# Kernel tuning notes

Hardware: AMD Instinct MI355X
Metric: run time of the kernel (lower is better)

## Reference

```python
import jax, jax.numpy as jnp
import numpy as np

EPS = 1e-5
NUM_HEADS = 32

def layer_norm(x, g, b):
    m = jnp.mean(x, axis=-1, keepdims=True)
    v = jnp.mean((x - m) ** 2, axis=-1, keepdims=True)
    return (x - m) * jax.lax.rsqrt(v + EPS) * g + b

def positional_encoding(S, E):
    pos = jnp.arange(S, dtype=jnp.float32)[:, None]
    div = jnp.exp(jnp.arange(0, E, 2, dtype=jnp.float32) * (-jnp.log(10000.0) / E))
    ang = pos * div  # [S, E/2]
    pe = jnp.zeros((S, E), jnp.float32)
    pe = pe.at[:, 0::2].set(jnp.sin(ang)).at[:, 1::2].set(jnp.cos(ang))
    return pe

def quantum_attention(x, phi_l):
    # QLayer circuit: RX(x_j + phi_j) per wire, CNOT ring, measure Z.
    # Heisenberg picture: <Z_i> = prod_{j<=i} cos(a_j) for i>=1,
    #                     <Z_0> = prod_{j>=1} cos(a_j), a_j = x_j + phi_j.
    B, S, E = x.shape
    dk = E // NUM_HEADS  # = 8 wires
    c = jnp.cos(x.reshape(B, S, NUM_HEADS, dk) + phi_l)  # per-wire <Z> factor
    pref = jnp.cumprod(c, axis=-1)                       # prod_{j<=i}
    out0 = jnp.prod(c[..., 1:], axis=-1)                 # wire 0
    q = jnp.concatenate([out0[..., None], pref[..., 1:]], axis=-1)
    q = q.reshape(B, S, E)
    scores = jax.nn.softmax(
        jnp.einsum('bse,bte->bst', q, q) / jnp.sqrt(jnp.float32(dk)), axis=-1)
    return jnp.einsum('bst,bte->bse', scores, q)

def quantum_ffn(x, theta_l, W1_l, b1_l, W2_l, b2_l):
    # QLayer: RX(x_i) then RY(theta_i) on |0>, product state => <Z_i>=cos(x_i)cos(theta_i)
    nq = theta_l.shape[0]  # 8; encoder only reads first nq features
    qm = jnp.cos(x[..., :nq]) * jnp.cos(theta_l)
    h = jax.nn.relu(qm @ W1_l + b1_l)
    return h @ W2_l + b2_l

def setup_inputs() -> dict:
    key = jax.random.key(0)
    ks = jax.random.split(key, 10)
    V, E, L, FF, NQ, NC = 32000, 256, 4, 1024, 8, 10
    B, S = 8, 2048
    return {
        'tokens': jax.random.randint(ks[0], (B, S), 0, V, dtype=jnp.int64)
            if jax.config.jax_enable_x64 else jax.random.randint(ks[0], (B, S), 0, V, dtype=jnp.int32),
        'emb': jax.random.normal(ks[1], (V, E), jnp.float32),
        'phi': jax.random.normal(ks[2], (L, NQ), jnp.float32),
        'theta': jax.random.normal(ks[3], (L, NQ), jnp.float32),
        'W1': jax.random.normal(ks[4], (L, NQ, FF), jnp.float32) * 0.1,
        'b1': jax.random.normal(ks[5], (L, FF), jnp.float32) * 0.1,
        'W2': jax.random.normal(ks[6], (L, FF, E), jnp.float32) * 0.05,
        'b2': jax.random.normal(ks[7], (L, E), jnp.float32) * 0.05,
        'g1': jnp.ones((L, E), jnp.float32),
        'beta1': jnp.zeros((L, E), jnp.float32),
        'g2': jnp.ones((L, E), jnp.float32),
        'beta2': jnp.zeros((L, E), jnp.float32),
        'Wc': jax.random.normal(ks[8], (E, NC), jnp.float32) * 0.05,
        'bc': jax.random.normal(ks[9], (NC,), jnp.float32) * 0.05,
    }

def reference(tokens, emb, phi, theta, W1, b1, W2, b2, g1, beta1, g2, beta2, Wc, bc):
    B, S = tokens.shape
    E = emb.shape[1]
    x = emb[tokens] + positional_encoding(S, E)
    for l in range(phi.shape[0]):  # fixed num_blocks loop
        a = quantum_attention(x, phi[l])
        x = layer_norm(x + a, g1[l], beta1[l])
        f = quantum_ffn(x, theta[l], W1[l], b1[l], W2[l], b2[l])
        x = layer_norm(x + f, g2[l], beta2[l])
    return jnp.mean(x, axis=1) @ Wc + bc
```

## Files before the change

### kernel.cpp

```cpp
#include <hip/hip_runtime.h>
#include <hip/hip_bf16.h>

#define B_ 8
#define S_ 2048
#define E_ 256
#define FF_ 1024
#define NQ_ 8
#define NC_ 10
#define BS_ (B_*S_)
#define NSPLIT 2
#define KVBLK 32

typedef __bf16 bf16x8 __attribute__((ext_vector_type(8)));
typedef float f32x4 __attribute__((ext_vector_type(4)));

#define MFMA16(a,b,c) __builtin_amdgcn_mfma_f32_16x16x32_bf16(a,b,c,0,0,0)

__global__ __launch_bounds__(256) void k_embed(const int* __restrict__ tokens,
                                               const float* __restrict__ emb,
                                               float* __restrict__ x) {
    int row = blockIdx.x;
    int e = threadIdx.x;
    int s = row & (S_ - 1);
    int tok = tokens[row];
    int i2 = e & ~1;
    float d = __expf((float)i2 * (-9.210340371976184f / 256.0f));
    float ang = (float)s * d;
    float pe = (e & 1) ? __cosf(ang) : __sinf(ang);
    x[(size_t)row * E_ + e] = emb[(size_t)tok * E_ + e] + pe;
}

__global__ __launch_bounds__(256) void k_qt(const float* __restrict__ x,
                                            const float* __restrict__ phi_l,
                                            __hip_bfloat16* __restrict__ qbf,
                                            __hip_bfloat16* __restrict__ qT) {
    __shared__ __align__(16) __bf16 tile[64][76];
    int t0 = blockIdx.x * 64, e0 = blockIdx.y * 64, b = blockIdx.z;
    int tid = threadIdx.x;
    float ph[8];
#pragma unroll
    for (int j = 0; j < 8; j++) ph[j] = phi_l[j];
#pragma unroll
    for (int k = 0; k < 2; k++) {
        int idx = k * 256 + tid;
        int r = idx >> 3, hh = idx & 7;
        const float* xp = x + ((size_t)b * S_ + t0 + r) * E_ + e0 + hh * 8;
        f32x4 x0 = *(const f32x4*)xp;
        f32x4 x1 = *(const f32x4*)(xp + 4);
        float c[8];
#pragma unroll
        for (int j = 0; j < 4; j++) {
            c[j]     = __cosf(x0[j] + ph[j]);
            c[4 + j] = __cosf(x1[j] + ph[4 + j]);
        }
        float q[8];
        float run = c[0];
#pragma unroll
        for (int i = 1; i < 8; i++) { run *= c[i]; q[i] = run; }
        float o0 = c[1];
#pragma unroll
        for (int i = 2; i < 8; i++) o0 *= c[i];
        q[0] = o0;
        bf16x8 v;
#pragma unroll
        for (int j = 0; j < 8; j++) v[j] = (__bf16)q[j];
        *(bf16x8*)(qbf + ((size_t)b * S_ + t0 + r) * E_ + e0 + hh * 8) = v;
        *(bf16x8*)&tile[r][hh * 8] = v;
    }
    __syncthreads();
#pragma unroll
    for (int k = 0; k < 2; k++) {
        int idx = k * 256 + tid;
        int el = idx >> 3, tc = idx & 7;
        bf16x8 v;
#pragma unroll
        for (int j = 0; j < 8; j++) v[j] = tile[tc * 8 + j][el];
        *(bf16x8*)(qT + ((size_t)b * E_ + e0 + el) * S_ + t0 + tc * 8) = v;
    }
}

__global__ __launch_bounds__(256, 2) void k_attn(const __hip_bfloat16* __restrict__ qbf,
                                                 const __hip_bfloat16* __restrict__ qT,
                                                 float* __restrict__ pacc,
                                                 float* __restrict__ pl) {
    __shared__ __align__(16) __bf16 ktile[KVBLK * 256];
    __shared__ __align__(16) __bf16 vtile[256 * 36];
    __shared__ __align__(16) __bf16 plds[2][32][36];
    __shared__ float redl[2][32][2];
    const float SCALE = 0.3535533905932738f;
    int bid  = blockIdx.x;
    int b    = bid & 7;
    int qt   = (bid >> 3) & 31;
    int z    = bid >> 8;
    int tid  = threadIdx.x;
    int wv   = tid >> 6;
    int lane = tid & 63;
    int r16  = lane & 15;
    int kg   = lane >> 4;
    int rg   = wv >> 1, eh = wv & 1;
    int qrow0 = qt * 64 + rg * 32;
    int ebase = eh * 128;

    bf16x8 aq[2][8];
#pragma unroll
    for (int qs = 0; qs < 2; qs++)
#pragma unroll
        for (int kk = 0; kk < 8; kk++)
            aq[qs][kk] = *(const bf16x8*)(qbf + ((size_t)b * S_ + qrow0 + qs * 16 + r16) * E_ + kk * 32 + kg * 8);

    f32x4 acc0[8], acc1[8];
#pragma unroll
    for (int cf = 0; cf < 8; cf++) { acc0[cf] = (f32x4){0.f,0.f,0.f,0.f}; acc1[cf] = (f32x4){0.f,0.f,0.f,0.f}; }
    float lrow0[4] = {0.f,0.f,0.f,0.f}, lrow1[4] = {0.f,0.f,0.f,0.f};

    int k0 = z * (S_ / NSPLIT);
    const int NT = (S_ / NSPLIT) / KVBLK;
    bf16x8 vst[4];

    auto issue_k = [&](int kb) {
#pragma unroll
        for (int c = 0; c < 4; c++) {
            int seg = wv * 4 + c;
            int r = seg * 2 + (lane >> 5);
            int ch = lane & 31;
            const __hip_bfloat16* src = qbf + ((size_t)b * S_ + kb + r) * E_ + ((ch ^ (r & 7)) * 8);
            __builtin_amdgcn_global_load_lds((const __attribute__((address_space(1))) void*)src,
                                             (__attribute__((address_space(3))) void*)(ktile + seg * 512),
                                             16, 0, 0);
        }
    };
    auto issue_v = [&](int kb) {
#pragma unroll
        for (int p = 0; p < 4; p++) {
            int slot = p * 256 + tid;
            vst[p] = *(const bf16x8*)(qT + ((size_t)b * E_ + (slot >> 2)) * S_ + kb + (slot & 3) * 8);
        }
    };
    auto write_v = [&]() {
#pragma unroll
        for (int p = 0; p < 4; p++) {
            int slot = p * 256 + tid;
            *(bf16x8*)&vtile[(slot >> 2) * 36 + (slot & 3) * 8] = vst[p];
        }
    };

    issue_k(k0);
    issue_v(k0);
    asm volatile("s_waitcnt vmcnt(0)" ::: "memory");
    write_v();
    __syncthreads();

    for (int kt = 0; kt < NT; kt++) {
        f32x4 s0 = (f32x4){0.f,0.f,0.f,0.f}, s1 = (f32x4){0.f,0.f,0.f,0.f};
#pragma unroll
        for (int kk = 0; kk < 8; kk++) {
            bf16x8 bk = *(const bf16x8*)&ktile[(eh * 16 + r16) * 256 + (((kk * 4 + kg) ^ (r16 & 7)) * 8)];
            s0 = MFMA16(aq[0][kk], bk, s0);
            s1 = MFMA16(aq[1][kk], bk, s1);
        }
#pragma unroll
        for (int i = 0; i < 4; i++) {
            float p0 = __expf(fmaf(s0[i], SCALE, -44.0f));
            float p1 = __expf(fmaf(s1[i], SCALE, -44.0f));
            plds[rg][kg * 4 + i][eh * 16 + r16]      = (__bf16)p0;
            plds[rg][16 + kg * 4 + i][eh * 16 + r16] = (__bf16)p1;
            lrow0[i] += p0;
            lrow1[i] += p1;
        }
        __syncthreads();
        bool more = (kt + 1 < NT);
        if (more) {
            int kn = k0 + (kt + 1) * KVBLK;
            issue_k(kn);
            issue_v(kn);
        }
        bf16x8 pa0 = *(const bf16x8*)&plds[rg][r16][kg * 8];
        bf16x8 pa1 = *(const bf16x8*)&plds[rg][16 + r16][kg * 8];
#pragma unroll
        for (int cf = 0; cf < 8; cf++) {
            bf16x8 bv = *(const bf16x8*)&vtile[(ebase + cf * 16 + r16) * 36 + kg * 8];
            acc0[cf] = MFMA16(pa0, bv, acc0[cf]);
            acc1[cf] = MFMA16(pa1, bv, acc1[cf]);
        }
        if (more) {
            asm volatile("s_waitcnt vmcnt(0)" ::: "memory");
            __syncthreads();
            write_v();
        }
    }

#pragma unroll
    for (int i = 0; i < 4; i++) {
#pragma unroll
        for (int m = 1; m <= 8; m <<= 1) {
            lrow0[i] += __shfl_xor(lrow0[i], m);
            lrow1[i] += __shfl_xor(lrow1[i], m);
        }
    }
    if (r16 == 0) {
#pragma unroll
        for (int i = 0; i < 4; i++) {
            redl[rg][kg * 4 + i][eh]      = lrow0[i];
            redl[rg][16 + kg * 4 + i][eh] = lrow1[i];
        }
    }
    __syncthreads();
    size_t prow0 = (size_t)z * BS_ + (size_t)b * S_ + qrow0;
    if (eh == 0 && r16 == 0) {
#pragma unroll
        for (int i = 0; i < 4; i++) {
            int q = kg * 4 + i;
            pl[prow0 + q]      = redl[rg][q][0] + redl[rg][q][1];
            pl[prow0 + 16 + q] = redl[rg][16 + q][0] + redl[rg][16 + q][1];
        }
    }
#pragma unroll
    for (int i = 0; i < 4; i++) {
#pragma unroll
        for (int cf = 0; cf < 8; cf++) {
            pacc[(prow0 + kg * 4 + i) * E_ + ebase + cf * 16 + r16]      = acc0[cf][i];
            pacc[(prow0 + 16 + kg * 4 + i) * E_ + ebase + cf * 16 + r16] = acc1[cf][i];
        }
    }
}

__global__ __launch_bounds__(256) void k_aln(const float* __restrict__ pacc,
                                             const float* __restrict__ pl,
                                             float* __restrict__ x,
                                             const float* __restrict__ g,
                                             const float* __restrict__ bb) {
    int wv = threadIdx.x >> 6, lane = threadIdx.x & 63;
    size_t row = (size_t)blockIdx.x * 4 + wv;
    float inv = 1.0f / (pl[row] + pl[BS_ + row]);
    f32x4 a0 = ((const f32x4*)(pacc + row * E_))[lane];
    f32x4 a1 = ((const f32x4*)(pacc + (size_t)BS_ * E_ + row * E_))[lane];
    f32x4 xv = ((const f32x4*)(x + row * E_))[lane];
    f32x4 v;
    float s = 0.f, sq = 0.f;
#pragma unroll
    for (int j = 0; j < 4; j++) {
        v[j] = xv[j] + (a0[j] + a1[j]) * inv;
        s += v[j]; sq += v[j] * v[j];
    }
#pragma unroll
    for (int m = 1; m <= 32; m <<= 1) { s += __shfl_xor(s, m); sq += __shfl_xor(sq, m); }
    float mean = s * (1.f / E_);
    float var = sq * (1.f / E_) - mean * mean;
    float rstd = rsqrtf(var + 1e-5f);
    f32x4 gv = ((const f32x4*)g)[lane];
    f32x4 bv = ((const f32x4*)bb)[lane];
    f32x4 o;
#pragma unroll
    for (int j = 0; j < 4; j++) o[j] = (v[j] - mean) * rstd * gv[j] + bv[j];
    ((f32x4*)(x + row * E_))[lane] = o;
}

__global__ __launch_bounds__(256) void k_w2t(const float* __restrict__ W2l,
                                             __hip_bfloat16* __restrict__ w2t) {
    __shared__ __align__(16) __bf16 tile[64][72];
    int k0 = blockIdx.x * 64, e0 = blockIdx.y * 64;
    int tid = threadIdx.x;
#pragma unroll
    for (int half = 0; half < 2; half++) {
        int r  = half * 32 + (tid >> 3);
        int c8 = (tid & 7) * 8;
        f32x4 v0 = *(const f32x4*)(W2l + (size_t)(k0 + r) * E_ + e0 + c8);
        f32x4 v1 = *(const f32x4*)(W2l + (size_t)(k0 + r) * E_ + e0 + c8 + 4);
#pragma unroll
        for (int j = 0; j < 4; j++) { tile[r][c8 + j] = (__bf16)v0[j]; tile[r][c8 + 4 + j] = (__bf16)v1[j]; }
    }
    __syncthreads();
#pragma unroll
    for (int half = 0; half < 2; half++) {
        int e  = half * 32 + (tid >> 3);
        int k8 = (tid & 7) * 8;
        bf16x8 v;
#pragma unroll
        for (int j = 0; j < 8; j++) v[j] = tile[k8 + j][e];
        *(bf16x8*)(w2t + (size_t)(e0 + e) * FF_ + k0 + k8) = v;
    }
}

__global__ __launch_bounds__(256) void k_ffn(const float* __restrict__ x,
                                             const float* __restrict__ theta_l,
                                             const float* __restrict__ W1l,
                                             const float* __restrict__ b1l,
                                             const __hip_bfloat16* __restrict__ w2t,
                                             const float* __restrict__ b2l,
                                             const float* __restrict__ g,
                                             const float* __restrict__ bb) {
    __shared__ __align__(16) __bf16 Bld[2][256 * 64];
    __shared__ __align__(16) __bf16 Ald[2][32 * 64];
    __shared__ float qmld[32][9];
    __shared__ float reds[32][4][2];
    int tid = threadIdx.x;
    int wv = tid >> 6, lane = tid & 63;
    int r16 = lane & 15, kg = lane >> 4;
    int rbase = blockIdx.x * 32;
    int ebQ = wv * 64;
    const int NT = FF_ / 64;

    {
        int r = tid >> 3, i = tid & 7;
        qmld[r][i] = __cosf(x[(size_t)(rbase + r) * E_ + i]) * __cosf(theta_l[i]);
    }

    f32x4 w[18];

    auto issue_B = [&](int kt, int buf) {
#pragma unroll
        for (int s = 0; s < 8; s++) {
            int seg = wv * 8 + s;
            int e = seg * 8 + (lane >> 3);
            int c = lane & 7;
            const __hip_bfloat16* src = w2t + (size_t)e * FF_ + kt * 64 + ((c ^ (e & 7)) * 8);
            __builtin_amdgcn_global_load_lds((const __attribute__((address_space(1))) void*)src,
                                             (__attribute__((address_space(3))) void*)(&Bld[buf][seg * 512]),
                                             16, 0, 0);
        }
    };
    auto load_W1 = [&](int kt) {
        int c = tid & 7;
        int k = kt * 64 + c * 8;
#pragma unroll
        for (int i = 0; i < 8; i++) {
            w[2 * i]     = *(const f32x4*)(W1l + (size_t)i * FF_ + k);
            w[2 * i + 1] = *(const f32x4*)(W1l + (size_t)i * FF_ + k + 4);
        }
        w[16] = *(const f32x4*)(b1l + k);
        w[17] = *(const f32x4*)(b1l + k + 4);
    };
    auto math_h = [&](int buf) {
        int r = tid >> 3, c = tid & 7;
        f32x4 h0 = w[16], h1 = w[17];
#pragma unroll
        for (int i = 0; i < 8; i++) {
            float qv = qmld[r][i];
#pragma unroll
            for (int j = 0; j < 4; j++) {
                h0[j] = fmaf(qv, w[2 * i][j], h0[j]);
                h1[j] = fmaf(qv, w[2 * i + 1][j], h1[j]);
            }
        }
        bf16x8 hv;
#pragma unroll
        for (int j = 0; j < 4; j++) {
            hv[j]     = (__bf16)fmaxf(h0[j], 0.f);
            hv[4 + j] = (__bf16)fmaxf(h1[j], 0.f);
        }
        *(bf16x8*)&Ald[buf][r * 64 + ((c ^ (r & 7)) * 8)] = hv;
    };

    issue_B(0, 0);
    load_W1(0);
    __syncthreads();
    math_h(0);
    __syncthreads();

    f32x4 acc[2][4];
#pragma unroll
    for (int qs = 0; qs < 2; qs++)
#pragma unroll
        for (int cf = 0; cf < 4; cf++) acc[qs][cf] = (f32x4){0.f, 0.f, 0.f, 0.f};

    for (int kt = 0; kt < NT; kt++) {
        int cur = kt & 1;
        bool more = (kt + 1 < NT);
        if (more) {
            issue_B(kt + 1, cur ^ 1);
            load_W1(kt + 1);
        }
        bf16x8 aq[2][2];
#pragma unroll
        for (int qs = 0; qs < 2; qs++)
#pragma unroll
            for (int kk = 0; kk < 2; kk++)
                aq[qs][kk] = *(const bf16x8*)&Ald[cur][(qs * 16 + r16) * 64 + (((kk * 4 + kg) ^ (r16 & 7)) * 8)];
#pragma unroll
        for (int cf = 0; cf < 4; cf++) {
            int e = ebQ + cf * 16 + r16;
#pragma unroll
            for (int kk = 0; kk < 2; kk++) {
                bf16x8 bv = *(const bf16x8*)&Bld[cur][e * 64 + (((kk * 4 + kg) ^ (e & 7)) * 8)];
                acc[0][cf] = MFMA16(aq[0][kk], bv, acc[0][cf]);
                acc[1][cf] = MFMA16(aq[1][kk], bv, acc[1][cf]);
            }
        }
        if (more) {
            math_h(cur ^ 1);
            __syncthreads();
        }
    }

    float sA[2][4] = {{0.f,0.f,0.f,0.f},{0.f,0.f,0.f,0.f}};
    float sQ[2][4] = {{0.f,0.f,0.f,0.f},{0.f,0.f,0.f,0.f}};
#pragma unroll
    for (int qs = 0; qs < 2; qs++)
#pragma unroll
        for (int cf = 0; cf < 4; cf++) {
            int e = ebQ + cf * 16 + r16;
            float b2v = b2l[e];
#pragma unroll
            for (int i = 0; i < 4; i++) {
                size_t orow = (size_t)rbase + qs * 16 + kg * 4 + i;
                float t = acc[qs][cf][i] + b2v + x[orow * E_ + e];
                acc[qs][cf][i] = t;
                sA[qs][i] += t; sQ[qs][i] += t * t;
            }
        }
#pragma unroll
    for (int qs = 0; qs < 2; qs++)
#pragma unroll
        for (int i = 0; i < 4; i++) {
#pragma unroll
            for (int m = 1; m <= 8; m <<= 1) {
                sA[qs][i] += __shfl_xor(sA[qs][i], m);
                sQ[qs][i] += __shfl_xor(sQ[qs][i], m);
            }
        }
    if (r16 == 0) {
#pragma unroll
        for (int qs = 0; qs < 2; qs++)
#pragma unroll
            for (int i = 0; i < 4; i++) {
                int row = qs * 16 + kg * 4 + i;
                reds[row][wv][0] = sA[qs][i];
                reds[row][wv][1] = sQ[qs][i];
            }
    }
    __syncthreads();
    float mean[2][4], rstd[2][4];
#pragma unroll
    for (int qs = 0; qs < 2; qs++)
#pragma unroll
        for (int i = 0; i < 4; i++) {
            int row = qs * 16 + kg * 4 + i;
            float S = reds[row][0][0] + reds[row][1][0] + reds[row][2][0] + reds[row][3][0];
            float Q = reds[row][0][1] + reds[row][1][1] + reds[row][2][1] + reds[row][3][1];
            mean[qs][i] = S * (1.f / E_);
            float var = Q * (1.f / E_) - mean[qs][i] * mean[qs][i];
            rstd[qs][i] = rsqrtf(var + 1e-5f);
        }
    float* xo = (float*)x;
#pragma unroll
    for (int qs = 0; qs < 2; qs++)
#pragma unroll
        for (int cf = 0; cf < 4; cf++) {
            int e = ebQ + cf * 16 + r16;
            float gv = g[e], bv = bb[e];
#pragma unroll
            for (int i = 0; i < 4; i++) {
                size_t orow = (size_t)rbase + qs * 16 + kg * 4 + i;
                xo[orow * E_ + e] = (acc[qs][cf][i] - mean[qs][i]) * rstd[qs][i] * gv + bv;
            }
        }
}

__global__ __launch_bounds__(256) void k_mean(const float* __restrict__ x, float* __restrict__ psum) {
    int c = blockIdx.x, b = blockIdx.y, e = threadIdx.x;
    float s = 0.f;
    size_t base = ((size_t)b * S_ + c * 128) * E_ + e;
    for (int r = 0; r < 128; r++) s += x[base + (size_t)r * E_];
    psum[(c * 8 + b) * E_ + e] = s;
}

__global__ __launch_bounds__(256) void k_mean2(const float* __restrict__ psum, float* __restrict__ xmean) {
    int idx = blockIdx.x * 256 + threadIdx.x;
    int b = idx >> 8, e = idx & 255;
    float s = 0.f;
    for (int c = 0; c < 16; c++) s += psum[(c * 8 + b) * E_ + e];
    xmean[idx] = s * (1.f / S_);
}

__global__ __launch_bounds__(128) void k_cls(const float* __restrict__ xmean,
                                             const float* __restrict__ Wc,
                                             const float* __restrict__ bc,
                                             float* __restrict__ outp) {
    int t = threadIdx.x;
    if (t >= B_ * NC_) return;
    int b = t / NC_, c = t % NC_;
    float s = bc[c];
    for (int e = 0; e < E_; e++) s += xmean[b * E_ + e] * Wc[e * NC_ + c];
    outp[t] = s;
}

extern "C" void kernel_launch(void* const* d_in, const int* in_sizes, int n_in,
                              void* d_out, int out_size, void* d_ws, size_t ws_size,
                              hipStream_t stream) {
    (void)in_sizes; (void)n_in; (void)out_size; (void)ws_size;
    const int*   tokens = (const int*)d_in[0];
    const float* emb    = (const float*)d_in[1];
    const float* phi    = (const float*)d_in[2];
    const float* theta  = (const float*)d_in[3];
    const float* W1     = (const float*)d_in[4];
    const float* b1     = (const float*)d_in[5];
    const float* W2     = (const float*)d_in[6];
    const float* b2     = (const float*)d_in[7];
    const float* g1     = (const float*)d_in[8];
    const float* beta1  = (const float*)d_in[9];
    const float* g2     = (const float*)d_in[10];
    const float* beta2  = (const float*)d_in[11];
    const float* Wc     = (const float*)d_in[12];
    const float* bc     = (const float*)d_in[13];
    float* outp = (float*)d_out;

    float* xbuf = (float*)d_ws;
    __hip_bfloat16* qbf = (__hip_bfloat16*)(xbuf + (size_t)BS_ * E_);
    __hip_bfloat16* qT  = qbf + (size_t)BS_ * E_;
    __hip_bfloat16* w2t = qT + (size_t)BS_ * E_;
    float* psum  = (float*)(w2t + (size_t)E_ * FF_);
    float* xmean = psum + 16 * 8 * E_;
    float* pl    = xmean + B_ * E_;
    float* pacc  = pl + NSPLIT * BS_;

    k_embed<<<BS_, 256, 0, stream>>>(tokens, emb, xbuf);

    for (int l = 0; l < 4; l++) {
        k_qt<<<dim3(S_ / 64, E_ / 64, B_), 256, 0, stream>>>(xbuf, phi + l * NQ_, qbf, qT);
        k_attn<<<(S_ / 64) * B_ * NSPLIT, 256, 0, stream>>>(qbf, qT, pacc, pl);
        k_aln<<<BS_ / 4, 256, 0, stream>>>(pacc, pl, xbuf, g1 + l * E_, beta1 + l * E_);
        k_w2t<<<dim3(FF_ / 64, E_ / 64), 256, 0, stream>>>(W2 + (size_t)l * FF_ * E_, w2t);
        k_ffn<<<BS_ / 32, 256, 0, stream>>>(xbuf, theta + l * NQ_,
                                            W1 + (size_t)l * NQ_ * FF_, b1 + (size_t)l * FF_,
                                            w2t, b2 + (size_t)l * E_,
                                            g2 + l * E_, beta2 + l * E_);
    }

    k_mean<<<dim3(16, B_), 256, 0, stream>>>(xbuf, psum);
    k_mean2<<<8, 256, 0, stream>>>(psum, xmean);
    k_cls<<<1, 128, 0, stream>>>(xmean, Wc, bc, outp);
}
```

Baseline: 464.5 us.

## Make attention KV split count runtime-selectable and raise attention occupancy hint

The attention kernel now splits the key range into nz chunks chosen at runtime (4 when the workspace can hold the larger partial buffers, else 2), doubling the grid so more blocks are in flight. The add-layernorm kernel sums a variable number of partial accumulators and row sums. Launch bounds for attention go from 2 to 4 waves per SIMD, which caps registers per thread and may cause spills given the large accumulator arrays. More splits also mean more partial-result memory traffic in the combine step.

```diff
diff --git a/kernel.cpp b/kernel.cpp
--- a/kernel.cpp
+++ b/kernel.cpp
@@ -8,7 +8,6 @@
 #define NQ_ 8
 #define NC_ 10
 #define BS_ (B_*S_)
-#define NSPLIT 2
 #define KVBLK 32
 
 typedef __bf16 bf16x8 __attribute__((ext_vector_type(8)));
@@ -79,10 +78,11 @@
     }
 }
 
-__global__ __launch_bounds__(256, 2) void k_attn(const __hip_bfloat16* __restrict__ qbf,
+__global__ __launch_bounds__(256, 4) void k_attn(const __hip_bfloat16* __restrict__ qbf,
                                                  const __hip_bfloat16* __restrict__ qT,
                                                  float* __restrict__ pacc,
-                                                 float* __restrict__ pl) {
+                                                 float* __restrict__ pl,
+                                                 int nz) {
     __shared__ __align__(16) __bf16 ktile[KVBLK * 256];
     __shared__ __align__(16) __bf16 vtile[256 * 36];
     __shared__ __align__(16) __bf16 plds[2][32][36];
@@ -113,8 +113,9 @@
     for (int cf = 0; cf < 8; cf++) { acc0[cf] = (f32x4){0.f,0.f,0.f,0.f}; acc1[cf] = (f32x4){0.f,0.f,0.f,0.f}; }
     float lrow0[4] = {0.f,0.f,0.f,0.f}, lrow1[4] = {0.f,0.f,0.f,0.f};
 
-    int k0 = z * (S_ / NSPLIT);
-    const int NT = (S_ / NSPLIT) / KVBLK;
+    int span = S_ / nz;
+    int k0 = z * span;
+    int NT = span / KVBLK;
     bf16x8 vst[4];
 
     auto issue_k = [&](int kb) {
@@ -228,18 +229,25 @@
                                              const float* __restrict__ pl,
                                              float* __restrict__ x,
                                              const float* __restrict__ g,
-                                             const float* __restrict__ bb) {
+                                             const float* __restrict__ bb,
+                                             int nz) {
     int wv = threadIdx.x >> 6, lane = threadIdx.x & 63;
     size_t row = (size_t)blockIdx.x * 4 + wv;
-    float inv = 1.0f / (pl[row] + pl[BS_ + row]);
-    f32x4 a0 = ((const f32x4*)(pacc + row * E_))[lane];
-    f32x4 a1 = ((const f32x4*)(pacc + (size_t)BS_ * E_ + row * E_))[lane];
+    float lsum = 0.f;
+    for (int zi = 0; zi < nz; zi++) lsum += pl[(size_t)zi * BS_ + row];
+    float inv = 1.0f / lsum;
+    f32x4 a = (f32x4){0.f, 0.f, 0.f, 0.f};
+    for (int zi = 0; zi < nz; zi++) {
+        f32x4 av = ((const f32x4*)(pacc + (size_t)zi * BS_ * E_ + row * E_))[lane];
+#pragma unroll
+        for (int j = 0; j < 4; j++) a[j] += av[j];
+    }
     f32x4 xv = ((const f32x4*)(x + row * E_))[lane];
     f32x4 v;
     float s = 0.f, sq = 0.f;
 #pragma unroll
     for (int j = 0; j < 4; j++) {
-        v[j] = xv[j] + (a0[j] + a1[j]) * inv;
+        v[j] = xv[j] + a[j] * inv;
         s += v[j]; sq += v[j] * v[j];
     }
 #pragma unroll
@@ -487,7 +495,7 @@
 extern "C" void kernel_launch(void* const* d_in, const int* in_sizes, int n_in,
                               void* d_out, int out_size, void* d_ws, size_t ws_size,
                               hipStream_t stream) {
-    (void)in_sizes; (void)n_in; (void)out_size; (void)ws_size;
+    (void)in_sizes; (void)n_in; (void)out_size;
     const int*   tokens = (const int*)d_in[0];
     const float* emb    = (const float*)d_in[1];
     const float* phi    = (const float*)d_in[2];
@@ -504,6 +512,11 @@
     const float* bc     = (const float*)d_in[13];
     float* outp = (float*)d_out;
 
+    size_t fixed = (size_t)BS_ * E_ * 4 + (size_t)BS_ * E_ * 2 * 2 + (size_t)E_ * FF_ * 2
+                 + (size_t)16 * 8 * E_ * 4 + (size_t)B_ * E_ * 4;
+    size_t per_z = (size_t)BS_ * 4 + (size_t)BS_ * E_ * 4;
+    int nz = (ws_size >= fixed + 4 * per_z + 4096) ? 4 : 2;
+
     float* xbuf = (float*)d_ws;
     __hip_bfloat16* qbf = (__hip_bfloat16*)(xbuf + (size_t)BS_ * E_);
     __hip_bfloat16* qT  = qbf + (size_t)BS_ * E_;
@@ -511,14 +524,14 @@
     float* psum  = (float*)(w2t + (size_t)E_ * FF_);
     float* xmean = psum + 16 * 8 * E_;
     float* pl    = xmean + B_ * E_;
-    float* pacc  = pl + NSPLIT * BS_;
+    float* pacc  = pl + (size_t)nz * BS_;
 
     k_embed<<<BS_, 256, 0, stream>>>(tokens, emb, xbuf);
 
     for (int l = 0; l < 4; l++) {
         k_qt<<<dim3(S_ / 64, E_ / 64, B_), 256, 0, stream>>>(xbuf, phi + l * NQ_, qbf, qT);
-        k_attn<<<(S_ / 64) * B_ * NSPLIT, 256, 0, stream>>>(qbf, qT, pacc, pl);
-        k_aln<<<BS_ / 4, 256, 0, stream>>>(pacc, pl, xbuf, g1 + l * E_, beta1 + l * E_);
+        k_attn<<<(S_ / 64) * B_ * nz, 256, 0, stream>>>(qbf, qT, pacc, pl, nz);
+        k_aln<<<BS_ / 4, 256, 0, stream>>>(pacc, pl, xbuf, g1 + l * E_, beta1 + l * E_, nz);
         k_w2t<<<dim3(FF_ / 64, E_ / 64), 256, 0, stream>>>(W2 + (size_t)l * FF_ * E_, w2t);
         k_ffn<<<BS_ / 32, 256, 0, stream>>>(xbuf, theta + l * NQ_,
                                             W1 + (size_t)l * NQ_ * FF_, b1 + (size_t)l * FF_,
```

Result: slower. 1.256 ms (+170.3%).

## Fuse attention-combine layernorm into FFN kernel and async-load V tiles into LDS

Applied to the files above, without the earlier changes.

Removes the separate k_aln kernel. The FFN kernel now reads the two split-K attention partials and the row sums, adds the residual, applies the first layernorm in registers, and derives the quantum FFN input from the normalized values. This saves a full read/write pass over the activations and one launch per layer. Separately, k_attn loads V tiles through global_load_lds into double-buffered, XOR-swizzled LDS instead of staging them in registers. That frees VGPRs and removes the LDS write step, at the cost of more shared memory per block, which may reduce occupancy.

```diff
diff --git a/kernel.cpp b/kernel.cpp
--- a/kernel.cpp
+++ b/kernel.cpp
@@ -84,7 +84,7 @@
                                                  float* __restrict__ pacc,
                                                  float* __restrict__ pl) {
     __shared__ __align__(16) __bf16 ktile[KVBLK * 256];
-    __shared__ __align__(16) __bf16 vtile[256 * 36];
+    __shared__ __align__(16) __bf16 vtile[2][256 * KVBLK];
     __shared__ __align__(16) __bf16 plds[2][32][36];
     __shared__ float redl[2][32][2];
     const float SCALE = 0.3535533905932738f;
@@ -113,9 +113,9 @@
     for (int cf = 0; cf < 8; cf++) { acc0[cf] = (f32x4){0.f,0.f,0.f,0.f}; acc1[cf] = (f32x4){0.f,0.f,0.f,0.f}; }
     float lrow0[4] = {0.f,0.f,0.f,0.f}, lrow1[4] = {0.f,0.f,0.f,0.f};
 
-    int k0 = z * (S_ / NSPLIT);
-    const int NT = (S_ / NSPLIT) / KVBLK;
-    bf16x8 vst[4];
+    constexpr int SPAN = S_ / NSPLIT;
+    constexpr int NT = SPAN / KVBLK;
+    int k0 = z * SPAN;
 
     auto issue_k = [&](int kb) {
 #pragma unroll
@@ -129,28 +129,26 @@
                                              16, 0, 0);
         }
     };
-    auto issue_v = [&](int kb) {
-#pragma unroll
-        for (int p = 0; p < 4; p++) {
-            int slot = p * 256 + tid;
-            vst[p] = *(const bf16x8*)(qT + ((size_t)b * E_ + (slot >> 2)) * S_ + kb + (slot & 3) * 8);
+    auto issue_v = [&](int kb, int buf) {
+#pragma unroll
+        for (int c = 0; c < 4; c++) {
+            int seg = wv * 4 + c;
+            int e = seg * 16 + (lane >> 2);
+            int ch = lane & 3;
+            const __hip_bfloat16* src = qT + ((size_t)b * E_ + e) * S_ + kb + ((ch ^ ((e >> 1) & 3)) * 8);
+            __builtin_amdgcn_global_load_lds((const __attribute__((address_space(1))) void*)src,
+                                             (__attribute__((address_space(3))) void*)(&vtile[buf][seg * 512]),
+                                             16, 0, 0);
         }
     };
-    auto write_v = [&]() {
-#pragma unroll
-        for (int p = 0; p < 4; p++) {
-            int slot = p * 256 + tid;
-            *(bf16x8*)&vtile[(slot >> 2) * 36 + (slot & 3) * 8] = vst[p];
-        }
-    };
 
     issue_k(k0);
-    issue_v(k0);
+    issue_v(k0, 0);
     asm volatile("s_waitcnt vmcnt(0)" ::: "memory");
-    write_v();
     __syncthreads();
 
     for (int kt = 0; kt < NT; kt++) {
+        int vcur = kt & 1;
         f32x4 s0 = (f32x4){0.f,0.f,0.f,0.f}, s1 = (f32x4){0.f,0.f,0.f,0.f};
 #pragma unroll
         for (int kk = 0; kk < 8; kk++) {
@@ -172,20 +170,20 @@
         if (more) {
             int kn = k0 + (kt + 1) * KVBLK;
             issue_k(kn);
-            issue_v(kn);
+            issue_v(kn, vcur ^ 1);
         }
         bf16x8 pa0 = *(const bf16x8*)&plds[rg][r16][kg * 8];
         bf16x8 pa1 = *(const bf16x8*)&plds[rg][16 + r16][kg * 8];
 #pragma unroll
         for (int cf = 0; cf < 8; cf++) {
-            bf16x8 bv = *(const bf16x8*)&vtile[(ebase + cf * 16 + r16) * 36 + kg * 8];
+            int vrow = ebase + cf * 16 + r16;
+            bf16x8 bv = *(const bf16x8*)&vtile[vcur][vrow * KVBLK + ((kg ^ ((vrow >> 1) & 3)) * 8)];
             acc0[cf] = MFMA16(pa0, bv, acc0[cf]);
             acc1[cf] = MFMA16(pa1, bv, acc1[cf]);
         }
         if (more) {
             asm volatile("s_waitcnt vmcnt(0)" ::: "memory");
             __syncthreads();
-            write_v();
         }
     }
 
@@ -222,37 +220,6 @@
             pacc[(prow0 + 16 + kg * 4 + i) * E_ + ebase + cf * 16 + r16] = acc1[cf][i];
         }
     }
-}
-
-__global__ __launch_bounds__(256) void k_aln(const float* __restrict__ pacc,
-                                             const float* __restrict__ pl,
-                                             float* __restrict__ x,
-                                             const float* __restrict__ g,
-                                             const float* __restrict__ bb) {
-    int wv = threadIdx.x >> 6, lane = threadIdx.x & 63;
-    size_t row = (size_t)blockIdx.x * 4 + wv;
-    float inv = 1.0f / (pl[row] + pl[BS_ + row]);
-    f32x4 a0 = ((const f32x4*)(pacc + row * E_))[lane];
-    f32x4 a1 = ((const f32x4*)(pacc + (size_t)BS_ * E_ + row * E_))[lane];
-    f32x4 xv = ((const f32x4*)(x + row * E_))[lane];
-    f32x4 v;
-    float s = 0.f, sq = 0.f;
-#pragma unroll
-    for (int j = 0; j < 4; j++) {
-        v[j] = xv[j] + (a0[j] + a1[j]) * inv;
-        s += v[j]; sq += v[j] * v[j];
-    }
-#pragma unroll
-    for (int m = 1; m <= 32; m <<= 1) { s += __shfl_xor(s, m); sq += __shfl_xor(sq, m); }
-    float mean = s * (1.f / E_);
-    float var = sq * (1.f / E_) - mean * mean;
-    float rstd = rsqrtf(var + 1e-5f);
-    f32x4 gv = ((const f32x4*)g)[lane];
-    f32x4 bv = ((const f32x4*)bb)[lane];
-    f32x4 o;
-#pragma unroll
-    for (int j = 0; j < 4; j++) o[j] = (v[j] - mean) * rstd * gv[j] + bv[j];
-    ((f32x4*)(x + row * E_))[lane] = o;
 }
 
 __global__ __launch_bounds__(256) void k_w2t(const float* __restrict__ W2l,
@@ -281,14 +248,18 @@
     }
 }
 
-__global__ __launch_bounds__(256) void k_ffn(const float* __restrict__ x,
+__global__ __launch_bounds__(256) void k_ffn(float* x,
+                                             const float* __restrict__ pacc,
+                                             const float* __restrict__ pl,
                                              const float* __restrict__ theta_l,
                                              const float* __restrict__ W1l,
                                              const float* __restrict__ b1l,
                                              const __hip_bfloat16* __restrict__ w2t,
                                              const float* __restrict__ b2l,
-                                             const float* __restrict__ g,
-                                             const float* __restrict__ bb) {
+                                             const float* __restrict__ g1,
+                                             const float* __restrict__ bt1,
+                                             const float* __restrict__ g2,
+                                             const float* __restrict__ bt2) {
     __shared__ __align__(16) __bf16 Bld[2][256 * 64];
     __shared__ __align__(16) __bf16 Ald[2][32 * 64];
     __shared__ float qmld[32][9];
@@ -300,13 +271,6 @@
     int ebQ = wv * 64;
     const int NT = FF_ / 64;
 
-    {
-        int r = tid >> 3, i = tid & 7;
-        qmld[r][i] = __cosf(x[(size_t)(rbase + r) * E_ + i]) * __cosf(theta_l[i]);
-    }
-
-    f32x4 w[18];
-
     auto issue_B = [&](int kt, int buf) {
 #pragma unroll
         for (int s = 0; s < 8; s++) {
@@ -319,6 +283,81 @@
                                              16, 0, 0);
         }
     };
+
+    issue_B(0, 0);
+
+    float linv[2][4];
+#pragma unroll
+    for (int qs = 0; qs < 2; qs++)
+#pragma unroll
+        for (int i = 0; i < 4; i++) {
+            int row = rbase + qs * 16 + kg * 4 + i;
+            linv[qs][i] = 1.0f / (pl[row] + pl[BS_ + row]);
+        }
+    f32x4 res[2][4];
+    float sA[2][4] = {{0.f,0.f,0.f,0.f},{0.f,0.f,0.f,0.f}};
+    float sQ[2][4] = {{0.f,0.f,0.f,0.f},{0.f,0.f,0.f,0.f}};
+#pragma unroll
+    for (int qs = 0; qs < 2; qs++)
+#pragma unroll
+        for (int cf = 0; cf < 4; cf++) {
+            int e = ebQ + cf * 16 + r16;
+#pragma unroll
+            for (int i = 0; i < 4; i++) {
+                size_t orow = (size_t)rbase + qs * 16 + kg * 4 + i;
+                float a = pacc[orow * E_ + e] + pacc[(size_t)BS_ * E_ + orow * E_ + e];
+                float v = x[orow * E_ + e] + a * linv[qs][i];
+                res[qs][cf][i] = v;
+                sA[qs][i] += v; sQ[qs][i] += v * v;
+            }
+        }
+#pragma unroll
+    for (int qs = 0; qs < 2; qs++)
+#pragma unroll
+        for (int i = 0; i < 4; i++) {
+#pragma unroll
+            for (int m = 1; m <= 8; m <<= 1) {
+                sA[qs][i] += __shfl_xor(sA[qs][i], m);
+                sQ[qs][i] += __shfl_xor(sQ[qs][i], m);
+            }
+        }
+    if (r16 == 0) {
+#pragma unroll
+        for (int qs = 0; qs < 2; qs++)
+#pragma unroll
+            for (int i = 0; i < 4; i++) {
+                int row = qs * 16 + kg * 4 + i;
+                reds[row][wv][0] = sA[qs][i];
+                reds[row][wv][1] = sQ[qs][i];
+            }
+    }
+    __syncthreads();
+#pragma unroll
+    for (int qs = 0; qs < 2; qs++)
+#pragma unroll
+        for (int i = 0; i < 4; i++) {
+            int row = qs * 16 + kg * 4 + i;
+            float S = reds[row][0][0] + reds[row][1][0] + reds[row][2][0] + reds[row][3][0];
+            float Q = reds[row][0][1] + reds[row][1][1] + reds[row][2][1] + reds[row][3][1];
+            float mean = S * (1.f / E_);
+            float var = Q * (1.f / E_) - mean * mean;
+            float rstd = rsqrtf(var + 1e-5f);
+#pragma unroll
+            for (int cf = 0; cf < 4; cf++) {
+                int e = ebQ + cf * 16 + r16;
+                res[qs][cf][i] = (res[qs][cf][i] - mean) * rstd * g1[e] + bt1[e];
+            }
+        }
+    if (wv == 0 && r16 < 8) {
+        float ct = __cosf(theta_l[r16]);
+#pragma unroll
+        for (int qs = 0; qs < 2; qs++)
+#pragma unroll
+            for (int i = 0; i < 4; i++)
+                qmld[qs * 16 + kg * 4 + i][r16] = __cosf(res[qs][0][i]) * ct;
+    }
+
+    f32x4 w[18];
     auto load_W1 = [&](int kt) {
         int c = tid & 7;
         int k = kt * 64 + c * 8;
@@ -351,7 +390,6 @@
         *(bf16x8*)&Ald[buf][r * 64 + ((c ^ (r & 7)) * 8)] = hv;
     };
 
-    issue_B(0, 0);
     load_W1(0);
     __syncthreads();
     math_h(0);
@@ -392,8 +430,10 @@
         }
     }
 
-    float sA[2][4] = {{0.f,0.f,0.f,0.f},{0.f,0.f,0.f,0.f}};
-    float sQ[2][4] = {{0.f,0.f,0.f,0.f},{0.f,0.f,0.f,0.f}};
+#pragma unroll
+    for (int qs = 0; qs < 2; qs++)
+#pragma unroll
+        for (int i = 0; i < 4; i++) { sA[qs][i] = 0.f; sQ[qs][i] = 0.f; }
 #pragma unroll
     for (int qs = 0; qs < 2; qs++)
 #pragma unroll
@@ -402,8 +442,7 @@
             float b2v = b2l[e];
 #pragma unroll
             for (int i = 0; i < 4; i++) {
-                size_t orow = (size_t)rbase + qs * 16 + kg * 4 + i;
-                float t = acc[qs][cf][i] + b2v + x[orow * E_ + e];
+                float t = acc[qs][cf][i] + b2v + res[qs][cf][i];
                 acc[qs][cf][i] = t;
                 sA[qs][i] += t; sQ[qs][i] += t * t;
             }
@@ -418,6 +457,7 @@
                 sQ[qs][i] += __shfl_xor(sQ[qs][i], m);
             }
         }
+    __syncthreads();
     if (r16 == 0) {
 #pragma unroll
         for (int qs = 0; qs < 2; qs++)
@@ -429,7 +469,6 @@
             }
     }
     __syncthreads();
-    float mean[2][4], rstd[2][4];
 #pragma unroll
     for (int qs = 0; qs < 2; qs++)
 #pragma unroll
@@ -437,21 +476,14 @@
             int row = qs * 16 + kg * 4 + i;
             float S = reds[row][0][0] + reds[row][1][0] + reds[row][2][0] + reds[row][3][0];
             float Q = reds[row][0][1] + reds[row][1][1] + reds[row][2][1] + reds[row][3][1];
-            mean[qs][i] = S * (1.f / E_);
-            float var = Q * (1.f / E_) - mean[qs][i] * mean[qs][i];
-            rstd[qs][i] = rsqrtf(var + 1e-5f);
-        }
-    float* xo = (float*)x;
-#pragma unroll
-    for (int qs = 0; qs < 2; qs++)
-#pragma unroll
-        for (int cf = 0; cf < 4; cf++) {
-            int e = ebQ + cf * 16 + r16;
-            float gv = g[e], bv = bb[e];
-#pragma unroll
-            for (int i = 0; i < 4; i++) {
-                size_t orow = (size_t)rbase + qs * 16 + kg * 4 + i;
-                xo[orow * E_ + e] = (acc[qs][cf][i] - mean[qs][i]) * rstd[qs][i] * gv + bv;
+            float mean = S * (1.f / E_);
+            float var = Q * (1.f / E_) - mean * mean;
+            float rstd = rsqrtf(var + 1e-5f);
+            size_t orow = (size_t)rbase + row;
+#pragma unroll
+            for (int cf = 0; cf < 4; cf++) {
+                int e = ebQ + cf * 16 + r16;
+                x[orow * E_ + e] = (acc[qs][cf][i] - mean) * rstd * g2[e] + bt2[e];
             }
         }
 }
@@ -511,18 +543,18 @@
     float* psum  = (float*)(w2t + (size_t)E_ * FF_);
     float* xmean = psum + 16 * 8 * E_;
     float* pl    = xmean + B_ * E_;
-    float* pacc  = pl + NSPLIT * BS_;
+    float* pacc  = pl + (size_t)NSPLIT * BS_;
 
     k_embed<<<BS_, 256, 0, stream>>>(tokens, emb, xbuf);
 
     for (int l = 0; l < 4; l++) {
         k_qt<<<dim3(S_ / 64, E_ / 64, B_), 256, 0, stream>>>(xbuf, phi + l * NQ_, qbf, qT);
         k_attn<<<(S_ / 64) * B_ * NSPLIT, 256, 0, stream>>>(qbf, qT, pacc, pl);
-        k_aln<<<BS_ / 4, 256, 0, stream>>>(pacc, pl, xbuf, g1 + l * E_, beta1 + l * E_);
         k_w2t<<<dim3(FF_ / 64, E_ / 64), 256, 0, stream>>>(W2 + (size_t)l * FF_ * E_, w2t);
-        k_ffn<<<BS_ / 32, 256, 0, stream>>>(xbuf, theta + l * NQ_,
+        k_ffn<<<BS_ / 32, 256, 0, stream>>>(xbuf, pacc, pl, theta + l * NQ_,
                                             W1 + (size_t)l * NQ_ * FF_, b1 + (size_t)l * FF_,
                                             w2t, b2 + (size_t)l * E_,
+                                            g1 + l * E_, beta1 + l * E_,
                                             g2 + l * E_, beta2 + l * E_);
     }
 
```

Result: slower. 526.6 us (+13.4%).
